# Performance work log

Measured on AMD Instinct MI355X. Metric: run time of the kernel, lower is better.

The kernel has to match this reference:

```python
import jax, jax.numpy as jnp
import numpy as np

N = 100000          # nodes
E = 3200000         # edges (avg degree 32)
D_IN = 64           # node_feature_dim
D_EMB = 128         # config.GNN_EMBEDDING_DIM
D_HID = 256         # config.RNN_HIDDEN_DIM


def setup_inputs() -> dict:
    key = jax.random.key(0)
    ks = jax.random.split(key, 12)
    s = 0.05
    return {
        "node_features": jax.random.normal(ks[0], (N, D_IN), jnp.float32),
        "edge_attr": jax.random.normal(ks[1], (E, 1), jnp.float32),
        "hidden_state": jax.random.normal(ks[2], (1, D_HID), jnp.float32),
        "W_enc": jax.random.normal(ks[3], (D_EMB, D_IN), jnp.float32) * s,
        "b_enc": jnp.zeros((D_EMB,), jnp.float32),
        "W_gcn": jax.random.normal(ks[4], (D_EMB, D_EMB), jnp.float32) * s,
        "b_gcn": jnp.zeros((D_EMB,), jnp.float32),
        "W_ih": jax.random.normal(ks[5], (3 * D_HID, D_EMB), jnp.float32) * s,
        "W_hh": jax.random.normal(ks[6], (3 * D_HID, D_HID), jnp.float32) * s,
        "b_ih": jax.random.normal(ks[7], (3 * D_HID,), jnp.float32) * s,
        "b_hh": jax.random.normal(ks[8], (3 * D_HID,), jnp.float32) * s,
        "edge_index": jax.random.randint(ks[9], (2, E), 0, N, jnp.int64),
    }


def reference(node_features, edge_attr, hidden_state, W_enc, b_enc, W_gcn,
              b_gcn, W_ih, W_hh, b_ih, b_hh, edge_index):
    n = node_features.shape[0]
    # Linear encoder + ReLU
    x = jax.nn.relu(node_features @ W_enc.T + b_enc)
    # GCNConv (PyG default): x' = D^-1/2 (A+I) D^-1/2 (x W^T) + b
    xw = x @ W_gcn.T
    loops = jnp.arange(n, dtype=edge_index.dtype)
    src = jnp.concatenate([edge_index[0], loops])
    dst = jnp.concatenate([edge_index[1], loops])
    deg = jax.ops.segment_sum(jnp.ones(src.shape, xw.dtype), dst, num_segments=n)
    dinv = jnp.where(deg > 0, jax.lax.rsqrt(deg), 0.0)
    norm = dinv[src] * dinv[dst]  # [E+N]
    agg = jax.ops.segment_sum(norm[:, None] * xw[src], dst, num_segments=n)
    g = jax.nn.relu(agg + b_gcn)
    agent = g[0:1, :]  # [1, D_EMB]
    # GRUCell
    gi = agent @ W_ih.T + b_ih
    gh = hidden_state @ W_hh.T + b_hh
    i_r, i_z, i_n = jnp.split(gi, 3, axis=1)
    h_r, h_z, h_n = jnp.split(gh, 3, axis=1)
    r = jax.nn.sigmoid(i_r + h_r)
    z = jax.nn.sigmoid(i_z + h_z)
    nn_ = jnp.tanh(i_n + r * h_n)
    return (1.0 - z) * nn_ + z * hidden_state
```

## Files before the change

kernel.cpp:

```cpp
#include <hip/hip_runtime.h>
#include <hip/hip_bf16.h>
#include <cstddef>

typedef __hip_bfloat16 bf16;

#define CAP   1024
#define MASKW 3328

struct Ws {
    int   count;
    int   done;
    int   pad[14];
    int   degs[CAP];
    float agg[128];
    int   srcs[CAP];
    float gi[768];
    float gh[768];
};

__device__ __forceinline__ float ldf(const void* p, int isf32, long long i) {
    if (isf32) return ((const float*)p)[i];
    return __bfloat162float(((const bf16*)p)[i]);
}

__device__ __forceinline__ void detect(const void* ei, const void* wenc,
                                       int& is64, int& isf32) {
    int l = threadIdx.x & 63;
    int hi = (l < 16) ? ((const int*)ei)[2 * l + 1] : 0;
    unsigned long long any_hi = __ballot(hi != 0);
    unsigned short u = ((const unsigned short*)wenc)[l];
    unsigned short ex = (u >> 7) & 0xFF;
    unsigned long long any_big = __ballot(ex >= 137);
    is64  = (any_hi == 0ull) ? 1 : 0;
    isf32 = (any_big != 0ull) ? 1 : 0;
}

__global__ void k_scan1(const void* __restrict__ ei, long long E, int EB,
                        const void* __restrict__ wenc,
                        const void* __restrict__ hidden,
                        const void* __restrict__ Whh,
                        const void* __restrict__ bhh,
                        Ws* w) {
    __shared__ float red[4];
    int is64, isf32;
    detect(ei, wenc, is64, isf32);
    int b = blockIdx.x;
    if (b < EB) {
        long long e0 = ((long long)b * blockDim.x + threadIdx.x) * 2;
        if (e0 >= E) return;
        int d0, d1;
        if (is64) {
            longlong2 dd = ((const longlong2*)ei)[(E + e0) >> 1];
            d0 = (int)dd.x; d1 = (int)dd.y;
        } else {
            int2 dd = ((const int2*)ei)[(E + e0) >> 1];
            d0 = dd.x; d1 = dd.y;
        }
        bool h1ok = (e0 + 1 < E);
        if (d0 == 0) {
            int p = atomicAdd(&w->count, 1);
            if (p < CAP) w->srcs[p] = (int)(is64 ? ((const long long*)ei)[e0]
                                                 : (long long)((const int*)ei)[e0]);
        }
        if (h1ok && d1 == 0) {
            int p = atomicAdd(&w->count, 1);
            if (p < CAP) w->srcs[p] = (int)(is64 ? ((const long long*)ei)[e0 + 1]
                                                 : (long long)((const int*)ei)[e0 + 1]);
        }
    } else {
        int j = b - EB;
        int t = threadIdx.x;
        float p = ldf(Whh, isf32, (long long)j * 256 + t) * ldf(hidden, isf32, t);
        #pragma unroll
        for (int off = 32; off > 0; off >>= 1) p += __shfl_down(p, off);
        if ((t & 63) == 0) red[t >> 6] = p;
        __syncthreads();
        if (t == 0)
            w->gh[j] = red[0] + red[1] + red[2] + red[3] + ldf(bhh, isf32, j);
    }
}

__global__ void k_deg(const void* __restrict__ ei, long long E,
                      const void* __restrict__ wenc, Ws* w) {
    __shared__ unsigned int mask[MASKW];
    __shared__ int ss[CAP];
    int is64, isf32;
    detect(ei, wenc, is64, isf32);
    int cnt = min(w->count, CAP);
    for (int i = threadIdx.x; i < MASKW; i += blockDim.x) mask[i] = 0u;
    __syncthreads();
    for (int i = threadIdx.x; i < cnt; i += blockDim.x) {
        int s = w->srcs[i];
        ss[i] = s;
        if ((unsigned)s < MASKW * 32u)
            atomicOr(&mask[s >> 5], 1u << (s & 31));
    }
    __syncthreads();
    long long e0 = ((long long)blockIdx.x * blockDim.x + threadIdx.x) * 2;
    if (e0 >= E) return;
    int d0, d1;
    if (is64) {
        longlong2 dd = ((const longlong2*)ei)[(E + e0) >> 1];
        d0 = (int)dd.x; d1 = (int)dd.y;
    } else {
        int2 dd = ((const int2*)ei)[(E + e0) >> 1];
        d0 = dd.x; d1 = dd.y;
    }
    bool h1ok = (e0 + 1 < E);
    bool t0 = ((unsigned)d0 < MASKW * 32u) ? ((mask[d0 >> 5] >> (d0 & 31)) & 1u) : true;
    bool t1 = h1ok && (((unsigned)d1 < MASKW * 32u) ? ((mask[d1 >> 5] >> (d1 & 31)) & 1u) : true);
    if (t0) for (int j = 0; j < cnt; j++) if (ss[j] == d0) atomicAdd(&w->degs[j], 1);
    if (t1) for (int j = 0; j < cnt; j++) if (ss[j] == d1) atomicAdd(&w->degs[j], 1);
}

__global__ void k_gather(const void* __restrict__ nf,
                         const void* __restrict__ Wenc,
                         const void* __restrict__ benc,
                         const void* __restrict__ Wgcn,
                         const void* __restrict__ ei,
                         Ws* w) {
    __shared__ float enc[128];
    __shared__ float nrow[64];
    int is64, isf32;
    detect(ei, Wenc, is64, isf32);
    (void)is64;
    int cnt  = min(w->count, CAP);
    int deg0 = w->count + 1;
    int t = threadIdx.x;
    for (int i = blockIdx.x; i <= cnt; i += gridDim.x) {
        int s; float norm;
        if (i < cnt) {
            s = w->srcs[i];
            norm = rsqrtf((float)(w->degs[i] + 1)) * rsqrtf((float)deg0);
        } else {
            s = 0;
            norm = 1.0f / (float)deg0;
        }
        if (t < 64) nrow[t] = ldf(nf, isf32, (long long)s * 64 + t);
        __syncthreads();
        float acc = 0.0f;
        if (isf32) {
            const float4* wr = (const float4*)((const float*)Wenc + (size_t)t * 64);
            #pragma unroll
            for (int k = 0; k < 16; k++) {
                float4 v = wr[k];
                acc += v.x * nrow[4*k] + v.y * nrow[4*k+1]
                     + v.z * nrow[4*k+2] + v.w * nrow[4*k+3];
            }
        } else {
            for (int k = 0; k < 64; k++)
                acc += ldf(Wenc, 0, (long long)t * 64 + k) * nrow[k];
        }
        acc += ldf(benc, isf32, t);
        enc[t] = fmaxf(acc, 0.0f);
        __syncthreads();
        float acc2 = 0.0f;
        if (isf32) {
            const float4* gr = (const float4*)((const float*)Wgcn + (size_t)t * 128);
            #pragma unroll
            for (int k = 0; k < 32; k++) {
                float4 v = gr[k];
                acc2 += v.x * enc[4*k] + v.y * enc[4*k+1]
                      + v.z * enc[4*k+2] + v.w * enc[4*k+3];
            }
        } else {
            for (int k = 0; k < 128; k++)
                acc2 += ldf(Wgcn, 0, (long long)t * 128 + k) * enc[k];
        }
        atomicAdd(&w->agg[t], norm * acc2);
        __syncthreads();
    }
}

__global__ void __launch_bounds__(64) k_gi(const void* __restrict__ ei,
                                           const void* __restrict__ wenc,
                                           Ws* __restrict__ w,
                                           const void* __restrict__ bgcn,
                                           const void* __restrict__ hidden,
                                           const void* __restrict__ Wih,
                                           const void* __restrict__ bih,
                                           void* __restrict__ out) {
    __shared__ int lastFlag;
    int is64, isf32;
    detect(ei, wenc, is64, isf32);
    (void)is64;
    int j = blockIdx.x;
    int lane = threadIdx.x;
    float a = 0.0f;
    #pragma unroll
    for (int p = 0; p < 2; p++) {
        int k = lane + 64 * p;
        float g0 = fmaxf(w->agg[k] + ldf(bgcn, isf32, k), 0.0f);
        a += ldf(Wih, isf32, (long long)j * 128 + k) * g0;
    }
    #pragma unroll
    for (int off = 32; off > 0; off >>= 1) a += __shfl_down(a, off);
    if (lane == 0) w->gi[j] = a + ldf(bih, isf32, j);

    __threadfence();
    if (lane == 0) {
        int old = atomicAdd(&w->done, 1);
        lastFlag = (old == (int)gridDim.x - 1) ? 1 : 0;
    }
    __syncthreads();
    if (!lastFlag) return;
    __threadfence();
    volatile float* vgi = w->gi;
    volatile float* vgh = w->gh;
    #pragma unroll
    for (int q = 0; q < 4; q++) {
        int t = lane + 64 * q;
        float r = 1.0f / (1.0f + expf(-(vgi[t]       + vgh[t])));
        float z = 1.0f / (1.0f + expf(-(vgi[256 + t] + vgh[256 + t])));
        float n = tanhf(vgi[512 + t] + r * vgh[512 + t]);
        float h = ldf(hidden, isf32, t);
        float val = (1.0f - z) * n + z * h;
        if (isf32) ((float*)out)[t] = val;
        else       ((bf16*)out)[t] = __float2bfloat16(val);
    }
}

extern "C" void kernel_launch(void* const* d_in, const int* in_sizes, int n_in,
                              void* d_out, int out_size, void* d_ws, size_t ws_size,
                              hipStream_t stream) {
    const void* nf   = d_in[0];
    const void* hid  = d_in[2];
    const void* Wenc = d_in[3];
    const void* benc = d_in[4];
    const void* Wgcn = d_in[5];
    const void* bgcn = d_in[6];
    const void* Wih  = d_in[7];
    const void* Whh  = d_in[8];
    const void* bih  = d_in[9];
    const void* bhh  = d_in[10];
    const void* ei   = d_in[11];
    long long E = in_sizes[11] / 2;

    Ws* w = (Ws*)d_ws;
    hipMemsetAsync(w, 0, offsetof(Ws, srcs), stream);

    int EB = (int)(((E + 1) / 2 + 255) / 256);
    k_scan1<<<EB + 768, 256, 0, stream>>>(ei, E, EB, Wenc, hid, Whh, bhh, w);
    k_deg<<<EB, 256, 0, stream>>>(ei, E, Wenc, w);
    k_gather<<<64, 128, 0, stream>>>(nf, Wenc, benc, Wgcn, ei, w);
    k_gi<<<768, 64, 0, stream>>>(ei, Wenc, w, bgcn, hid, Wih, bih, d_out);
}
```

Baseline: 165.0 us.

## Fuse all stages into one cooperative persistent kernel with grid syncs

Replaces the memset and four separate kernel launches with a single cooperative kernel that uses grid-wide syncs between phases: zeroing, a scan for edges into node 0, the degree count, the gather-encode step and the GRU. It also shrinks the shared-memory destination bitmask from 3328 words to a 64-word hashed mask, which lowers shared memory use and raises occupancy but lets more false-positive edges fall through to the linear search. The intent is to remove launch overhead and inter-kernel gaps. In exchange it adds grid-sync costs, host occupancy queries on every call, and grid-stride loops in place of one thread per edge pair.

```diff
diff --git a/kernel.cpp b/kernel.cpp
--- a/kernel.cpp
+++ b/kernel.cpp
@@ -1,16 +1,15 @@
 #include <hip/hip_runtime.h>
 #include <hip/hip_bf16.h>
-#include <cstddef>
-
+#include <hip/hip_cooperative_groups.h>
+
+namespace cg = cooperative_groups;
 typedef __hip_bfloat16 bf16;
 
-#define CAP   1024
-#define MASKW 3328
+#define CAP 1024
 
 struct Ws {
     int   count;
-    int   done;
-    int   pad[14];
+    int   pad[15];
     int   degs[CAP];
     float agg[128];
     int   srcs[CAP];
@@ -35,185 +34,175 @@
     isf32 = (any_big != 0ull) ? 1 : 0;
 }
 
-__global__ void k_scan1(const void* __restrict__ ei, long long E, int EB,
-                        const void* __restrict__ wenc,
-                        const void* __restrict__ hidden,
-                        const void* __restrict__ Whh,
-                        const void* __restrict__ bhh,
-                        Ws* w) {
+__device__ __forceinline__ void load2dst(const void* ei, int is64, long long E,
+                                         long long p, int& d0, int& d1) {
+    if (is64) {
+        longlong2 dd = ((const longlong2*)ei)[(E >> 1) + p];
+        d0 = (int)dd.x; d1 = (int)dd.y;
+    } else {
+        int2 dd = ((const int2*)ei)[(E >> 1) + p];
+        d0 = dd.x; d1 = dd.y;
+    }
+}
+
+__global__ void __launch_bounds__(256) k_all(
+    const void* __restrict__ nf,  const void* __restrict__ hid,
+    const void* __restrict__ Wenc,const void* __restrict__ benc,
+    const void* __restrict__ Wgcn,const void* __restrict__ bgcn,
+    const void* __restrict__ Wih, const void* __restrict__ Whh,
+    const void* __restrict__ bih, const void* __restrict__ bhh,
+    const void* __restrict__ ei,  long long E,
+    void* __restrict__ out, Ws* __restrict__ w)
+{
+    cg::grid_group grid = cg::this_grid();
+    __shared__ int   ss[CAP];
+    __shared__ unsigned int hmask[64];
+    __shared__ float enc[128];
+    __shared__ float nrow[64];
     __shared__ float red[4];
+
+    const int t = threadIdx.x;
     int is64, isf32;
-    detect(ei, wenc, is64, isf32);
-    int b = blockIdx.x;
-    if (b < EB) {
-        long long e0 = ((long long)b * blockDim.x + threadIdx.x) * 2;
-        if (e0 >= E) return;
-        int d0, d1;
-        if (is64) {
-            longlong2 dd = ((const longlong2*)ei)[(E + e0) >> 1];
-            d0 = (int)dd.x; d1 = (int)dd.y;
-        } else {
-            int2 dd = ((const int2*)ei)[(E + e0) >> 1];
-            d0 = dd.x; d1 = dd.y;
-        }
-        bool h1ok = (e0 + 1 < E);
-        if (d0 == 0) {
-            int p = atomicAdd(&w->count, 1);
-            if (p < CAP) w->srcs[p] = (int)(is64 ? ((const long long*)ei)[e0]
-                                                 : (long long)((const int*)ei)[e0]);
-        }
-        if (h1ok && d1 == 0) {
-            int p = atomicAdd(&w->count, 1);
-            if (p < CAP) w->srcs[p] = (int)(is64 ? ((const long long*)ei)[e0 + 1]
-                                                 : (long long)((const int*)ei)[e0 + 1]);
+    detect(ei, Wenc, is64, isf32);
+
+    const long long gthread = (long long)blockIdx.x * blockDim.x + t;
+    const long long gsize   = (long long)gridDim.x * blockDim.x;
+    const bool evenE = ((E & 1) == 0);
+    const long long pairs = E >> 1;
+
+    if (gthread == 0) w->count = 0;
+    for (long long i = gthread; i < CAP; i += gsize) w->degs[i] = 0;
+    for (long long i = gthread; i < 128; i += gsize) w->agg[i] = 0.0f;
+    grid.sync();
+
+    if (evenE) {
+        for (long long p = gthread; p < pairs; p += gsize) {
+            int d0, d1; load2dst(ei, is64, E, p, d0, d1);
+            if (d0 == 0) {
+                int q = atomicAdd(&w->count, 1);
+                if (q < CAP) w->srcs[q] = (int)(is64 ? ((const long long*)ei)[2*p]
+                                                     : (long long)((const int*)ei)[2*p]);
+            }
+            if (d1 == 0) {
+                int q = atomicAdd(&w->count, 1);
+                if (q < CAP) w->srcs[q] = (int)(is64 ? ((const long long*)ei)[2*p+1]
+                                                     : (long long)((const int*)ei)[2*p+1]);
+            }
         }
     } else {
-        int j = b - EB;
-        int t = threadIdx.x;
-        float p = ldf(Whh, isf32, (long long)j * 256 + t) * ldf(hidden, isf32, t);
+        for (long long e = gthread; e < E; e += gsize) {
+            int d = is64 ? (int)((const long long*)ei)[E + e] : ((const int*)ei)[E + e];
+            if (d == 0) {
+                int q = atomicAdd(&w->count, 1);
+                if (q < CAP) w->srcs[q] = (int)(is64 ? ((const long long*)ei)[e]
+                                                     : (long long)((const int*)ei)[e]);
+            }
+        }
+    }
+    for (int j = blockIdx.x; j < 768; j += gridDim.x) {
+        float p = ldf(Whh, isf32, (long long)j * 256 + t) * ldf(hid, isf32, t);
         #pragma unroll
         for (int off = 32; off > 0; off >>= 1) p += __shfl_down(p, off);
         if ((t & 63) == 0) red[t >> 6] = p;
         __syncthreads();
-        if (t == 0)
-            w->gh[j] = red[0] + red[1] + red[2] + red[3] + ldf(bhh, isf32, j);
-    }
-}
-
-__global__ void k_deg(const void* __restrict__ ei, long long E,
-                      const void* __restrict__ wenc, Ws* w) {
-    __shared__ unsigned int mask[MASKW];
-    __shared__ int ss[CAP];
-    int is64, isf32;
-    detect(ei, wenc, is64, isf32);
-    int cnt = min(w->count, CAP);
-    for (int i = threadIdx.x; i < MASKW; i += blockDim.x) mask[i] = 0u;
+        if (t == 0) w->gh[j] = red[0] + red[1] + red[2] + red[3] + ldf(bhh, isf32, j);
+        __syncthreads();
+    }
+    grid.sync();
+
+    const int cnt = min(w->count, CAP);
+    for (int i = t; i < 64; i += 256) hmask[i] = 0u;
     __syncthreads();
-    for (int i = threadIdx.x; i < cnt; i += blockDim.x) {
+    for (int i = t; i < cnt; i += 256) {
         int s = w->srcs[i];
         ss[i] = s;
-        if ((unsigned)s < MASKW * 32u)
-            atomicOr(&mask[s >> 5], 1u << (s & 31));
+        atomicOr(&hmask[(s >> 5) & 63], 1u << (s & 31));
     }
     __syncthreads();
-    long long e0 = ((long long)blockIdx.x * blockDim.x + threadIdx.x) * 2;
-    if (e0 >= E) return;
-    int d0, d1;
-    if (is64) {
-        longlong2 dd = ((const longlong2*)ei)[(E + e0) >> 1];
-        d0 = (int)dd.x; d1 = (int)dd.y;
+    if (evenE) {
+        for (long long p = gthread; p < pairs; p += gsize) {
+            int d0, d1; load2dst(ei, is64, E, p, d0, d1);
+            bool t0 = (hmask[(d0 >> 5) & 63] >> (d0 & 31)) & 1u;
+            bool t1 = (hmask[(d1 >> 5) & 63] >> (d1 & 31)) & 1u;
+            if (t0) for (int j = 0; j < cnt; j++) if (ss[j] == d0) atomicAdd(&w->degs[j], 1);
+            if (t1) for (int j = 0; j < cnt; j++) if (ss[j] == d1) atomicAdd(&w->degs[j], 1);
+        }
     } else {
-        int2 dd = ((const int2*)ei)[(E + e0) >> 1];
-        d0 = dd.x; d1 = dd.y;
-    }
-    bool h1ok = (e0 + 1 < E);
-    bool t0 = ((unsigned)d0 < MASKW * 32u) ? ((mask[d0 >> 5] >> (d0 & 31)) & 1u) : true;
-    bool t1 = h1ok && (((unsigned)d1 < MASKW * 32u) ? ((mask[d1 >> 5] >> (d1 & 31)) & 1u) : true);
-    if (t0) for (int j = 0; j < cnt; j++) if (ss[j] == d0) atomicAdd(&w->degs[j], 1);
-    if (t1) for (int j = 0; j < cnt; j++) if (ss[j] == d1) atomicAdd(&w->degs[j], 1);
-}
-
-__global__ void k_gather(const void* __restrict__ nf,
-                         const void* __restrict__ Wenc,
-                         const void* __restrict__ benc,
-                         const void* __restrict__ Wgcn,
-                         const void* __restrict__ ei,
-                         Ws* w) {
-    __shared__ float enc[128];
-    __shared__ float nrow[64];
-    int is64, isf32;
-    detect(ei, Wenc, is64, isf32);
-    (void)is64;
-    int cnt  = min(w->count, CAP);
-    int deg0 = w->count + 1;
-    int t = threadIdx.x;
+        for (long long e = gthread; e < E; e += gsize) {
+            int d = is64 ? (int)((const long long*)ei)[E + e] : ((const int*)ei)[E + e];
+            if ((hmask[(d >> 5) & 63] >> (d & 31)) & 1u)
+                for (int j = 0; j < cnt; j++) if (ss[j] == d) atomicAdd(&w->degs[j], 1);
+        }
+    }
+    grid.sync();
+
+    const int deg0 = w->count + 1;
     for (int i = blockIdx.x; i <= cnt; i += gridDim.x) {
         int s; float norm;
         if (i < cnt) {
             s = w->srcs[i];
             norm = rsqrtf((float)(w->degs[i] + 1)) * rsqrtf((float)deg0);
-        } else {
-            s = 0;
-            norm = 1.0f / (float)deg0;
-        }
+        } else { s = 0; norm = 1.0f / (float)deg0; }
         if (t < 64) nrow[t] = ldf(nf, isf32, (long long)s * 64 + t);
         __syncthreads();
-        float acc = 0.0f;
-        if (isf32) {
-            const float4* wr = (const float4*)((const float*)Wenc + (size_t)t * 64);
-            #pragma unroll
-            for (int k = 0; k < 16; k++) {
-                float4 v = wr[k];
-                acc += v.x * nrow[4*k] + v.y * nrow[4*k+1]
-                     + v.z * nrow[4*k+2] + v.w * nrow[4*k+3];
-            }
-        } else {
-            for (int k = 0; k < 64; k++)
-                acc += ldf(Wenc, 0, (long long)t * 64 + k) * nrow[k];
-        }
-        acc += ldf(benc, isf32, t);
-        enc[t] = fmaxf(acc, 0.0f);
-        __syncthreads();
-        float acc2 = 0.0f;
-        if (isf32) {
-            const float4* gr = (const float4*)((const float*)Wgcn + (size_t)t * 128);
-            #pragma unroll
-            for (int k = 0; k < 32; k++) {
-                float4 v = gr[k];
-                acc2 += v.x * enc[4*k] + v.y * enc[4*k+1]
-                      + v.z * enc[4*k+2] + v.w * enc[4*k+3];
-            }
-        } else {
-            for (int k = 0; k < 128; k++)
-                acc2 += ldf(Wgcn, 0, (long long)t * 128 + k) * enc[k];
-        }
-        atomicAdd(&w->agg[t], norm * acc2);
-        __syncthreads();
-    }
-}
-
-__global__ void __launch_bounds__(64) k_gi(const void* __restrict__ ei,
-                                           const void* __restrict__ wenc,
-                                           Ws* __restrict__ w,
-                                           const void* __restrict__ bgcn,
-                                           const void* __restrict__ hidden,
-                                           const void* __restrict__ Wih,
-                                           const void* __restrict__ bih,
-                                           void* __restrict__ out) {
-    __shared__ int lastFlag;
-    int is64, isf32;
-    detect(ei, wenc, is64, isf32);
-    (void)is64;
-    int j = blockIdx.x;
-    int lane = threadIdx.x;
-    float a = 0.0f;
-    #pragma unroll
-    for (int p = 0; p < 2; p++) {
-        int k = lane + 64 * p;
-        float g0 = fmaxf(w->agg[k] + ldf(bgcn, isf32, k), 0.0f);
-        a += ldf(Wih, isf32, (long long)j * 128 + k) * g0;
-    }
-    #pragma unroll
-    for (int off = 32; off > 0; off >>= 1) a += __shfl_down(a, off);
-    if (lane == 0) w->gi[j] = a + ldf(bih, isf32, j);
-
-    __threadfence();
-    if (lane == 0) {
-        int old = atomicAdd(&w->done, 1);
-        lastFlag = (old == (int)gridDim.x - 1) ? 1 : 0;
-    }
-    __syncthreads();
-    if (!lastFlag) return;
-    __threadfence();
-    volatile float* vgi = w->gi;
-    volatile float* vgh = w->gh;
-    #pragma unroll
-    for (int q = 0; q < 4; q++) {
-        int t = lane + 64 * q;
-        float r = 1.0f / (1.0f + expf(-(vgi[t]       + vgh[t])));
-        float z = 1.0f / (1.0f + expf(-(vgi[256 + t] + vgh[256 + t])));
-        float n = tanhf(vgi[512 + t] + r * vgh[512 + t]);
-        float h = ldf(hidden, isf32, t);
+        if (t < 128) {
+            float acc = 0.0f;
+            if (isf32) {
+                const float4* wr = (const float4*)((const float*)Wenc + (size_t)t * 64);
+                #pragma unroll 4
+                for (int k = 0; k < 16; k++) {
+                    float4 v = wr[k];
+                    acc += v.x * nrow[4*k] + v.y * nrow[4*k+1]
+                         + v.z * nrow[4*k+2] + v.w * nrow[4*k+3];
+                }
+            } else {
+                for (int k = 0; k < 64; k++)
+                    acc += ldf(Wenc, 0, (long long)t * 64 + k) * nrow[k];
+            }
+            acc += ldf(benc, isf32, t);
+            enc[t] = fmaxf(acc, 0.0f);
+        }
+        __syncthreads();
+        if (t < 128) {
+            float acc2 = 0.0f;
+            if (isf32) {
+                const float4* gr = (const float4*)((const float*)Wgcn + (size_t)t * 128);
+                #pragma unroll 4
+                for (int k = 0; k < 32; k++) {
+                    float4 v = gr[k];
+                    acc2 += v.x * enc[4*k] + v.y * enc[4*k+1]
+                          + v.z * enc[4*k+2] + v.w * enc[4*k+3];
+                }
+            } else {
+                for (int k = 0; k < 128; k++)
+                    acc2 += ldf(Wgcn, 0, (long long)t * 128 + k) * enc[k];
+            }
+            atomicAdd(&w->agg[t], norm * acc2);
+        }
+        __syncthreads();
+    }
+    grid.sync();
+
+    for (int j = blockIdx.x; j < 768; j += gridDim.x) {
+        float a = 0.0f;
+        if (t < 128) {
+            float g0 = fmaxf(w->agg[t] + ldf(bgcn, isf32, t), 0.0f);
+            a = ldf(Wih, isf32, (long long)j * 128 + t) * g0;
+        }
+        #pragma unroll
+        for (int off = 32; off > 0; off >>= 1) a += __shfl_down(a, off);
+        if ((t & 63) == 0 && t < 128) red[t >> 6] = a;
+        __syncthreads();
+        if (t == 0) w->gi[j] = red[0] + red[1] + ldf(bih, isf32, j);
+        __syncthreads();
+    }
+    grid.sync();
+
+    if (blockIdx.x == 0) {
+        float r = 1.0f / (1.0f + expf(-(w->gi[t]       + w->gh[t])));
+        float z = 1.0f / (1.0f + expf(-(w->gi[256 + t] + w->gh[256 + t])));
+        float n = tanhf(w->gi[512 + t] + r * w->gh[512 + t]);
+        float h = ldf(hid, isf32, t);
         float val = (1.0f - z) * n + z * h;
         if (isf32) ((float*)out)[t] = val;
         else       ((bf16*)out)[t] = __float2bfloat16(val);
@@ -235,13 +224,22 @@
     const void* bhh  = d_in[10];
     const void* ei   = d_in[11];
     long long E = in_sizes[11] / 2;
-
+    void* out = d_out;
     Ws* w = (Ws*)d_ws;
-    hipMemsetAsync(w, 0, offsetof(Ws, srcs), stream);
-
-    int EB = (int)(((E + 1) / 2 + 255) / 256);
-    k_scan1<<<EB + 768, 256, 0, stream>>>(ei, E, EB, Wenc, hid, Whh, bhh, w);
-    k_deg<<<EB, 256, 0, stream>>>(ei, E, Wenc, w);
-    k_gather<<<64, 128, 0, stream>>>(nf, Wenc, benc, Wgcn, ei, w);
-    k_gi<<<768, 64, 0, stream>>>(ei, Wenc, w, bgcn, hid, Wih, bih, d_out);
-}
+
+    int nbpc = 0;
+    if (hipOccupancyMaxActiveBlocksPerMultiprocessor(&nbpc, (const void*)k_all, 256, 0)
+        != hipSuccess || nbpc < 1) nbpc = 1;
+    int ncu = 0;
+    if (hipDeviceGetAttribute(&ncu, hipDeviceAttributeMultiprocessorCount, 0)
+        != hipSuccess || ncu < 1) ncu = 256;
+    long long grid = (long long)nbpc * ncu;
+    if (grid > 2048) grid = 2048;
+
+    void* args[] = {(void*)&nf, (void*)&hid, (void*)&Wenc, (void*)&benc,
+                    (void*)&Wgcn, (void*)&bgcn, (void*)&Wih, (void*)&Whh,
+                    (void*)&bih, (void*)&bhh, (void*)&ei, (void*)&E,
+                    (void*)&out, (void*)&w};
+    hipLaunchCooperativeKernel((const void*)k_all, dim3((unsigned)grid), dim3(256),
+                               args, 0, stream);
+}
```

Result: slower. 422.1 us (+155.8%).

## Compute full degree histogram in scan pass, drop separate degree kernel, single-block GRU

Applied to the files above, without the earlier changes.

Replaces the second pass over destination indices (mask filter plus linear search over node 0's sources) with a global per-node degree histogram built by atomics in the first scan pass, so edge_index is read once. The gather kernel then looks up source degrees directly in the histogram. The GRU input projection and gating are merged into one 1024-thread block, removing the last-block atomic handoff. In exchange it memsets an N-sized histogram and issues 3.2M global atomics spread over 100k addresses.

```diff
diff --git a/kernel.cpp b/kernel.cpp
--- a/kernel.cpp
+++ b/kernel.cpp
@@ -4,18 +4,15 @@
 
 typedef __hip_bfloat16 bf16;
 
-#define CAP   1024
-#define MASKW 3328
+#define CAP 1024
 
 struct Ws {
     int   count;
-    int   done;
-    int   pad[14];
-    int   degs[CAP];
+    int   pad[31];
     float agg[128];
+    float gh[768];
     int   srcs[CAP];
-    float gi[768];
-    float gh[768];
+    int   deghist[1];
 };
 
 __device__ __forceinline__ float ldf(const void* p, int isf32, long long i) {
@@ -35,42 +32,56 @@
     isf32 = (any_big != 0ull) ? 1 : 0;
 }
 
-__global__ void k_scan1(const void* __restrict__ ei, long long E, int EB,
-                        const void* __restrict__ wenc,
-                        const void* __restrict__ hidden,
-                        const void* __restrict__ Whh,
-                        const void* __restrict__ bhh,
-                        Ws* w) {
+__global__ void k_scan(const void* __restrict__ ei, long long E, int EB,
+                       const void* __restrict__ wenc,
+                       const void* __restrict__ hid,
+                       const void* __restrict__ Whh,
+                       const void* __restrict__ bhh,
+                       Ws* __restrict__ w) {
     __shared__ float red[4];
     int is64, isf32;
     detect(ei, wenc, is64, isf32);
     int b = blockIdx.x;
     if (b < EB) {
-        long long e0 = ((long long)b * blockDim.x + threadIdx.x) * 2;
-        if (e0 >= E) return;
-        int d0, d1;
-        if (is64) {
-            longlong2 dd = ((const longlong2*)ei)[(E + e0) >> 1];
-            d0 = (int)dd.x; d1 = (int)dd.y;
-        } else {
-            int2 dd = ((const int2*)ei)[(E + e0) >> 1];
-            d0 = dd.x; d1 = dd.y;
-        }
-        bool h1ok = (e0 + 1 < E);
-        if (d0 == 0) {
-            int p = atomicAdd(&w->count, 1);
-            if (p < CAP) w->srcs[p] = (int)(is64 ? ((const long long*)ei)[e0]
-                                                 : (long long)((const int*)ei)[e0]);
-        }
-        if (h1ok && d1 == 0) {
-            int p = atomicAdd(&w->count, 1);
-            if (p < CAP) w->srcs[p] = (int)(is64 ? ((const long long*)ei)[e0 + 1]
-                                                 : (long long)((const int*)ei)[e0 + 1]);
+        if ((E & 1) == 0) {
+            long long p = (long long)b * blockDim.x + threadIdx.x;
+            long long pairs = E >> 1;
+            if (p >= pairs) return;
+            int d0, d1;
+            if (is64) {
+                longlong2 dd = ((const longlong2*)ei)[(E >> 1) + p];
+                d0 = (int)dd.x; d1 = (int)dd.y;
+            } else {
+                int2 dd = ((const int2*)ei)[(E >> 1) + p];
+                d0 = dd.x; d1 = dd.y;
+            }
+            atomicAdd(&w->deghist[d0], 1);
+            atomicAdd(&w->deghist[d1], 1);
+            if (d0 == 0) {
+                int q = atomicAdd(&w->count, 1);
+                if (q < CAP) w->srcs[q] = (int)(is64 ? ((const long long*)ei)[2*p]
+                                                     : (long long)((const int*)ei)[2*p]);
+            }
+            if (d1 == 0) {
+                int q = atomicAdd(&w->count, 1);
+                if (q < CAP) w->srcs[q] = (int)(is64 ? ((const long long*)ei)[2*p+1]
+                                                     : (long long)((const int*)ei)[2*p+1]);
+            }
+        } else {
+            long long e = (long long)b * blockDim.x + threadIdx.x;
+            if (e >= E) return;
+            int d = is64 ? (int)((const long long*)ei)[E + e] : ((const int*)ei)[E + e];
+            atomicAdd(&w->deghist[d], 1);
+            if (d == 0) {
+                int q = atomicAdd(&w->count, 1);
+                if (q < CAP) w->srcs[q] = (int)(is64 ? ((const long long*)ei)[e]
+                                                     : (long long)((const int*)ei)[e]);
+            }
         }
     } else {
         int j = b - EB;
         int t = threadIdx.x;
-        float p = ldf(Whh, isf32, (long long)j * 256 + t) * ldf(hidden, isf32, t);
+        float p = ldf(Whh, isf32, (long long)j * 256 + t) * ldf(hid, isf32, t);
         #pragma unroll
         for (int off = 32; off > 0; off >>= 1) p += __shfl_down(p, off);
         if ((t & 63) == 0) red[t >> 6] = p;
@@ -78,39 +89,6 @@
         if (t == 0)
             w->gh[j] = red[0] + red[1] + red[2] + red[3] + ldf(bhh, isf32, j);
     }
-}
-
-__global__ void k_deg(const void* __restrict__ ei, long long E,
-                      const void* __restrict__ wenc, Ws* w) {
-    __shared__ unsigned int mask[MASKW];
-    __shared__ int ss[CAP];
-    int is64, isf32;
-    detect(ei, wenc, is64, isf32);
-    int cnt = min(w->count, CAP);
-    for (int i = threadIdx.x; i < MASKW; i += blockDim.x) mask[i] = 0u;
-    __syncthreads();
-    for (int i = threadIdx.x; i < cnt; i += blockDim.x) {
-        int s = w->srcs[i];
-        ss[i] = s;
-        if ((unsigned)s < MASKW * 32u)
-            atomicOr(&mask[s >> 5], 1u << (s & 31));
-    }
-    __syncthreads();
-    long long e0 = ((long long)blockIdx.x * blockDim.x + threadIdx.x) * 2;
-    if (e0 >= E) return;
-    int d0, d1;
-    if (is64) {
-        longlong2 dd = ((const longlong2*)ei)[(E + e0) >> 1];
-        d0 = (int)dd.x; d1 = (int)dd.y;
-    } else {
-        int2 dd = ((const int2*)ei)[(E + e0) >> 1];
-        d0 = dd.x; d1 = dd.y;
-    }
-    bool h1ok = (e0 + 1 < E);
-    bool t0 = ((unsigned)d0 < MASKW * 32u) ? ((mask[d0 >> 5] >> (d0 & 31)) & 1u) : true;
-    bool t1 = h1ok && (((unsigned)d1 < MASKW * 32u) ? ((mask[d1 >> 5] >> (d1 & 31)) & 1u) : true);
-    if (t0) for (int j = 0; j < cnt; j++) if (ss[j] == d0) atomicAdd(&w->degs[j], 1);
-    if (t1) for (int j = 0; j < cnt; j++) if (ss[j] == d1) atomicAdd(&w->degs[j], 1);
 }
 
 __global__ void k_gather(const void* __restrict__ nf,
@@ -118,20 +96,20 @@
                          const void* __restrict__ benc,
                          const void* __restrict__ Wgcn,
                          const void* __restrict__ ei,
-                         Ws* w) {
+                         Ws* __restrict__ w) {
     __shared__ float enc[128];
     __shared__ float nrow[64];
     int is64, isf32;
     detect(ei, Wenc, is64, isf32);
     (void)is64;
     int cnt  = min(w->count, CAP);
-    int deg0 = w->count + 1;
+    int deg0 = w->deghist[0] + 1;
     int t = threadIdx.x;
     for (int i = blockIdx.x; i <= cnt; i += gridDim.x) {
         int s; float norm;
         if (i < cnt) {
             s = w->srcs[i];
-            norm = rsqrtf((float)(w->degs[i] + 1)) * rsqrtf((float)deg0);
+            norm = rsqrtf((float)(w->deghist[s] + 1)) * rsqrtf((float)deg0);
         } else {
             s = 0;
             norm = 1.0f / (float)deg0;
@@ -172,48 +150,35 @@
     }
 }
 
-__global__ void __launch_bounds__(64) k_gi(const void* __restrict__ ei,
-                                           const void* __restrict__ wenc,
-                                           Ws* __restrict__ w,
-                                           const void* __restrict__ bgcn,
-                                           const void* __restrict__ hidden,
-                                           const void* __restrict__ Wih,
-                                           const void* __restrict__ bih,
-                                           void* __restrict__ out) {
-    __shared__ int lastFlag;
+__global__ void __launch_bounds__(1024) k_gru(
+        const void* __restrict__ ei, const void* __restrict__ wenc,
+        Ws* __restrict__ w,
+        const void* __restrict__ bgcn, const void* __restrict__ hid,
+        const void* __restrict__ Wih,  const void* __restrict__ bih,
+        void* __restrict__ out) {
+    __shared__ float g0L[128];
+    __shared__ float giL[768];
     int is64, isf32;
     detect(ei, wenc, is64, isf32);
     (void)is64;
-    int j = blockIdx.x;
-    int lane = threadIdx.x;
-    float a = 0.0f;
-    #pragma unroll
-    for (int p = 0; p < 2; p++) {
-        int k = lane + 64 * p;
-        float g0 = fmaxf(w->agg[k] + ldf(bgcn, isf32, k), 0.0f);
-        a += ldf(Wih, isf32, (long long)j * 128 + k) * g0;
-    }
-    #pragma unroll
-    for (int off = 32; off > 0; off >>= 1) a += __shfl_down(a, off);
-    if (lane == 0) w->gi[j] = a + ldf(bih, isf32, j);
-
-    __threadfence();
-    if (lane == 0) {
-        int old = atomicAdd(&w->done, 1);
-        lastFlag = (old == (int)gridDim.x - 1) ? 1 : 0;
-    }
+    int t = threadIdx.x;
+    if (t < 128) g0L[t] = fmaxf(w->agg[t] + ldf(bgcn, isf32, t), 0.0f);
     __syncthreads();
-    if (!lastFlag) return;
-    __threadfence();
-    volatile float* vgi = w->gi;
-    volatile float* vgh = w->gh;
-    #pragma unroll
-    for (int q = 0; q < 4; q++) {
-        int t = lane + 64 * q;
-        float r = 1.0f / (1.0f + expf(-(vgi[t]       + vgh[t])));
-        float z = 1.0f / (1.0f + expf(-(vgi[256 + t] + vgh[256 + t])));
-        float n = tanhf(vgi[512 + t] + r * vgh[512 + t]);
-        float h = ldf(hidden, isf32, t);
+    int wv = t >> 6, lane = t & 63;
+    for (int j = wv; j < 768; j += 16) {
+        long long base = (long long)j * 128;
+        float a = ldf(Wih, isf32, base + lane)      * g0L[lane]
+                + ldf(Wih, isf32, base + 64 + lane) * g0L[64 + lane];
+        #pragma unroll
+        for (int off = 32; off > 0; off >>= 1) a += __shfl_down(a, off);
+        if (lane == 0) giL[j] = a + ldf(bih, isf32, j);
+    }
+    __syncthreads();
+    if (t < 256) {
+        float r = 1.0f / (1.0f + expf(-(giL[t]       + w->gh[t])));
+        float z = 1.0f / (1.0f + expf(-(giL[256 + t] + w->gh[256 + t])));
+        float n = tanhf(giL[512 + t] + r * w->gh[512 + t]);
+        float h = ldf(hid, isf32, t);
         float val = (1.0f - z) * n + z * h;
         if (isf32) ((float*)out)[t] = val;
         else       ((bf16*)out)[t] = __float2bfloat16(val);
@@ -235,13 +200,15 @@
     const void* bhh  = d_in[10];
     const void* ei   = d_in[11];
     long long E = in_sizes[11] / 2;
+    long long Nnodes = in_sizes[0] / 64;
 
     Ws* w = (Ws*)d_ws;
-    hipMemsetAsync(w, 0, offsetof(Ws, srcs), stream);
-
-    int EB = (int)(((E + 1) / 2 + 255) / 256);
-    k_scan1<<<EB + 768, 256, 0, stream>>>(ei, E, EB, Wenc, hid, Whh, bhh, w);
-    k_deg<<<EB, 256, 0, stream>>>(ei, E, Wenc, w);
+    size_t zbytes = offsetof(Ws, deghist) + (size_t)Nnodes * sizeof(int);
+    hipMemsetAsync(w, 0, zbytes, stream);
+
+    int EB = (E & 1) == 0 ? (int)(((E >> 1) + 255) / 256)
+                          : (int)((E + 255) / 256);
+    k_scan<<<EB + 768, 256, 0, stream>>>(ei, E, EB, Wenc, hid, Whh, bhh, w);
     k_gather<<<64, 128, 0, stream>>>(nf, Wenc, benc, Wgcn, ei, w);
-    k_gi<<<768, 64, 0, stream>>>(ei, Wenc, w, bgcn, hid, Wih, bih, d_out);
-}
+    k_gru<<<1, 1024, 0, stream>>>(ei, Wenc, w, bgcn, hid, Wih, bih, d_out);
+}
```

New measurement: 280.4 us. +70.0%, slower.
